# Performance work log

Measured on AMD Instinct MI355X. Metric: run time of the kernel, lower is better.

Reference implementation:

```python
import jax, jax.numpy as jnp
import numpy as np

TAU = 0.2
ALPHA = 0.8
LAM_POS = 1.5  # extrapolation lambda (hard positives)
EPS = 1e-8


def _cosine_sim(e):
    # torch F.cosine_similarity with eps=1e-8 norm clamping
    n = jnp.maximum(jnp.linalg.norm(e, axis=1), EPS)
    return (e @ e.T) / (n[:, None] * n[None, :])


def setup_inputs() -> dict:
    key = jax.random.key(0)
    N, D = 4096, 128
    emb = jax.random.normal(key, (N, D), dtype=jnp.float32)
    k = jnp.arange(N // 2, dtype=jnp.int32)
    i, j = 2 * k, 2 * k + 1
    # disjoint positive pairs, both orientations (matches symmetric set semantics)
    pp = jnp.concatenate([jnp.stack([i, j], 1), jnp.stack([j, i], 1)], 0)
    return {"embeddings": emb, "positive_pairs": pp, "stage_train": 1}


def reference(embeddings, positive_pairs, stage_train):
    N = embeddings.shape[0]
    pi, pj = positive_pairs[:, 0], positive_pairs[:, 1]
    Mp = jnp.zeros((N, N), dtype=bool).at[pi, pj].set(True)  # symmetric (both dirs in pairs)
    eye = jnp.eye(N, dtype=bool)
    Mn = (~eye) & (~Mp)  # negative pair mask

    # hard positive extrapolation: 1.5*e_i - 0.5*e_j (pairs disjoint -> order-free)
    hard_pos = jnp.zeros_like(embeddings).at[pi].set(
        LAM_POS * embeddings[pi] + (1.0 - LAM_POS) * embeddings[pj])

    # hard negative interpolation: loop over negatives in row-major order, last write
    idx = jnp.arange(N, dtype=jnp.int32)
    posmat = idx[:, None] * N + idx[None, :]          # enumeration position of pair (i,j)
    A = jnp.where(Mn, posmat, -1)
    col_max, col_arg = A.max(axis=0), A.argmax(axis=0)  # m as second element of (i,m)
    row_max, row_arg = A.max(axis=1), A.argmax(axis=1)  # m as first element of (m,j)
    partner = jnp.where(col_max > row_max, col_arg, row_arg)
    hard_neg = 0.5 * (embeddings + embeddings[partner])

    sim = _cosine_sim(embeddings)
    sim = jnp.where(Mp, _cosine_sim(hard_pos), jnp.where(Mn, _cosine_sim(hard_neg), sim))

    # contrastive loss with quantile hard mining
    mask = eye | Mp
    exp_sim = jnp.exp(sim / TAU)
    exp_masked = jnp.where(mask, 0.0, exp_sim)
    pos_ij = exp_sim[pi, pj]
    pos_ji = exp_sim[pj, pi]
    ei = exp_masked[pi]  # [2P, N]
    ej = exp_masked[pj]
    if stage_train:
        ti = jnp.quantile(ei, ALPHA, axis=1, keepdims=True)
        tj = jnp.quantile(ej, ALPHA, axis=1, keepdims=True)
        si = jnp.where(ei >= ti, ei, 0.0).sum(axis=1)
        sj = jnp.where(ej >= tj, ej, 0.0).sum(axis=1)
    else:
        si = ei.sum(axis=1)
        sj = ej.sum(axis=1)
    loss_ij = -jnp.log(pos_ij / (pos_ij + si))
    loss_ji = -jnp.log(pos_ji / (pos_ji + sj))
    num_pairs = positive_pairs.shape[0]
    return (loss_ij + loss_ji).sum() / (2 * num_pairs)
```

## Files before the change

### kernel.cpp

```cpp
#include <hip/hip_runtime.h>
#include <hip/hip_bf16.h>
#include <math.h>

#define D 128
#define INV_TAU 5.0f
#define BINS 512
#define BSTRIDE 520
#define CCAP 384

typedef short bf16x8 __attribute__((ext_vector_type(8)));
typedef float f32x4 __attribute__((ext_vector_type(4)));

__global__ void scatter_pos(const int* __restrict__ pp, int* __restrict__ pos,
                            float* __restrict__ out, int K) {
    int k = blockIdx.x * blockDim.x + threadIdx.x;
    if (k == 0) *out = 0.0f;
    if (k < K) pos[pp[2 * k]] = pp[2 * k + 1];
}

__global__ void partner_kernel(const int* __restrict__ pos, int* __restrict__ partner,
                               int N) {
    int r = blockIdx.x * blockDim.x + threadIdx.x;
    if (r >= N) return;
    int posr = pos[r];
    int jmax = -1;
    for (int j = N - 1; j >= 0; --j) {
        if (j != r && j != posr) { jmax = j; break; }
    }
    int imax = -1;
    for (int i = N - 1; i >= 0; --i) {
        if (i != r && pos[i] != r) { imax = i; break; }
    }
    long long rowm = (jmax >= 0) ? (long long)r * N + jmax : -1;
    long long colm = (imax >= 0) ? (long long)imax * N + r : -1;
    partner[r] = (colm > rowm) ? (imax < 0 ? 0 : imax) : (jmax < 0 ? 0 : jmax);
}

__global__ void prep_kernel(const float* __restrict__ emb, const int* __restrict__ partner,
                            const int* __restrict__ pp, __hip_bfloat16* __restrict__ hnn,
                            float* __restrict__ hpn, int N) {
    int b = blockIdx.x, d = threadIdx.x;
    float h;
    int outrow;
    bool isHn = (b < N);
    if (isHn) {
        int p = partner[b];
        h = 0.5f * (emb[b * D + d] + emb[p * D + d]);
        outrow = b;
    } else {
        int k = b - N;
        int a = pp[2 * k], bb = pp[2 * k + 1];
        h = 1.5f * emb[a * D + d] - 0.5f * emb[bb * D + d];
        outrow = a;
    }
    float ss = h * h;
#pragma unroll
    for (int off = 32; off > 0; off >>= 1) ss += __shfl_down(ss, off);
    __shared__ float tmp[2];
    if ((d & 63) == 0) tmp[d >> 6] = ss;
    __syncthreads();
    float inv = 1.0f / fmaxf(sqrtf(tmp[0] + tmp[1]), 1e-8f);
    if (isHn)
        hnn[outrow * D + d] = __float2bfloat16(h * inv);
    else
        hpn[outrow * D + d] = h * inv;
}

__global__ __launch_bounds__(1024, 4) void fused_gram_select(
    const __hip_bfloat16* __restrict__ hnn, const int* __restrict__ pos,
    const int* __restrict__ stage, float* __restrict__ s_out, int N, int q) {
    __shared__ unsigned hist[16 * BSTRIDE];
    __shared__ float rowSum[16];
    __shared__ float tVal_s[16];
    __shared__ int tBin_s[16], tRem_s[16], cCnt[16], pos_s[16];

    int tid = threadIdx.x;
    int wave = tid >> 6, lane = tid & 63;
    int quad = lane >> 4, l15 = lane & 15;
    int rowBase = blockIdx.x * 16;
    int st = stage[0];

    for (int i = tid; i < 16 * BSTRIDE; i += 1024) hist[i] = 0;
    if (tid < 16) {
        rowSum[tid] = 0.0f;
        cCnt[tid] = 0;
        tVal_s[tid] = -1e31f;
        pos_s[tid] = pos[rowBase + tid];
    }
    __syncthreads();

    const short* hs = (const short*)hnn;
    bf16x8 afrag[4];
#pragma unroll
    for (int kk = 0; kk < 4; ++kk)
        afrag[kk] = *(const bf16x8*)&hs[(rowBase + l15) * D + kk * 32 + quad * 8];

    float simv[16][4];
#pragma unroll
    for (int t = 0; t < 16; ++t) {
        int colBase = (wave * 16 + t) * 16;
        bf16x8 bfrag[4];
#pragma unroll
        for (int kk = 0; kk < 4; ++kk)
            bfrag[kk] = *(const bf16x8*)&hs[(colBase + l15) * D + kk * 32 + quad * 8];
        f32x4 acc = {0.f, 0.f, 0.f, 0.f};
#pragma unroll
        for (int kk = 0; kk < 4; ++kk)
            acc = __builtin_amdgcn_mfma_f32_16x16x32_bf16(afrag[kk], bfrag[kk], acc, 0, 0, 0);
        int c = colBase + l15;
#pragma unroll
        for (int rg = 0; rg < 4; ++rg) {
            int rloc = quad * 4 + rg;
            int r = rowBase + rloc;
            float v = acc[rg];
            bool masked = (c == r) || (c == pos_s[rloc]);
            v = masked ? -1e30f : v;
            simv[t][rg] = v;
            if (st) {
                int bin = (int)floorf((v + 1.0f) * (float)(BINS / 2));
                bin = max(0, min(BINS - 1, bin));
                atomicAdd(&hist[rloc * BSTRIDE + bin], 1u);
            }
        }
    }
    __syncthreads();

    if (st) {
        int rloc = wave;
        int base = lane * (BINS / 64);
        unsigned p = 0;
#pragma unroll
        for (int b = 0; b < BINS / 64; ++b) p += hist[rloc * BSTRIDE + base + b];
        unsigned incl = p;
#pragma unroll
        for (int off = 1; off < 64; off <<= 1) {
            unsigned nb = __shfl_up(incl, off);
            if (lane >= off) incl += nb;
        }
        unsigned excl = incl - p;
        unsigned uq = (unsigned)q;
        if (uq >= excl && uq < excl + p) {
            unsigned rem = uq - excl, acc2 = 0;
            int b = 0;
            for (; b < BINS / 64; ++b) {
                unsigned h = hist[rloc * BSTRIDE + base + b];
                if (acc2 + h > rem) break;
                acc2 += h;
            }
            tBin_s[rloc] = base + b;
            tRem_s[rloc] = (int)(rem - acc2);
        }
    } else {
        if (tid < 16) { tBin_s[tid] = -1; tRem_s[tid] = 0; }
    }
    __syncthreads();

    float* cand = (float*)hist;
    float partial[4] = {0.f, 0.f, 0.f, 0.f};
#pragma unroll
    for (int t = 0; t < 16; ++t) {
#pragma unroll
        for (int rg = 0; rg < 4; ++rg) {
            int rloc = quad * 4 + rg;
            float v = simv[t][rg];
            int tb = tBin_s[rloc];
            int bin = 0;
            if (st) {
                bin = (int)floorf((v + 1.0f) * (float)(BINS / 2));
                bin = max(0, min(BINS - 1, bin));
            }
            if (bin > tb) {
                partial[rg] += __expf(v * INV_TAU);
            } else if (bin == tb) {
                int ix = atomicAdd(&cCnt[rloc], 1);
                if (ix < CCAP) cand[rloc * BSTRIDE + ix] = v;
            }
        }
    }
#pragma unroll
    for (int rg = 0; rg < 4; ++rg) {
        float v = partial[rg];
        v += __shfl_xor(v, 1);
        v += __shfl_xor(v, 2);
        v += __shfl_xor(v, 4);
        v += __shfl_xor(v, 8);
        if (l15 == 0) atomicAdd(&rowSum[quad * 4 + rg], v);
    }
    __syncthreads();

    {
        int rloc = wave;
        int m = min(cCnt[rloc], CCAP);
        int rem = tRem_s[rloc];
        for (int i = lane; i < m; i += 64) {
            float v = cand[rloc * BSTRIDE + i];
            int less = 0, eq = 0;
            for (int j = 0; j < m; ++j) {
                float w = cand[rloc * BSTRIDE + j];
                less += (w < v);
                eq += (w == v);
            }
            if (less <= rem && rem < less + eq) tVal_s[rloc] = v;
        }
    }
    __syncthreads();

    {
        int rloc = wave;
        int m = min(cCnt[rloc], CCAP);
        float tv = tVal_s[rloc];
        float csum = 0.0f;
        for (int i = lane; i < m; i += 64) {
            float v = cand[rloc * BSTRIDE + i];
            if (v >= tv) csum += __expf(v * INV_TAU);
        }
#pragma unroll
        for (int off = 1; off < 64; off <<= 1) csum += __shfl_xor(csum, off);
        if (lane == 0) s_out[rowBase + rloc] = rowSum[rloc] + csum;
    }
}

__global__ __launch_bounds__(1024) void loss_kernel(const float* __restrict__ hpn,
                                                    const float* __restrict__ s,
                                                    const int* __restrict__ pp,
                                                    float* __restrict__ out, int K,
                                                    float scale) {
    int wave = threadIdx.x >> 6, lane = threadIdx.x & 63;
    int k = blockIdx.x * 16 + wave;
    float part = 0.0f;
    if (k < K) {
        int a = pp[2 * k], b = pp[2 * k + 1];
        float dsum = hpn[a * D + lane] * hpn[b * D + lane] +
                     hpn[a * D + lane + 64] * hpn[b * D + lane + 64];
#pragma unroll
        for (int off = 32; off > 0; off >>= 1) dsum += __shfl_down(dsum, off);
        if (lane == 0) {
            float p = __expf(dsum * INV_TAU);
            part = log1pf(s[a] / p) + log1pf(s[b] / p);
        }
    }
    __shared__ float red[16];
    if (lane == 0) red[wave] = part;
    __syncthreads();
    if (threadIdx.x == 0) {
        float tot = 0.0f;
#pragma unroll
        for (int w = 0; w < 16; ++w) tot += red[w];
        atomicAdd(out, tot * scale);
    }
}

extern "C" void kernel_launch(void* const* d_in, const int* in_sizes, int n_in,
                              void* d_out, int out_size, void* d_ws, size_t ws_size,
                              hipStream_t stream) {
    const float* emb = (const float*)d_in[0];
    const int* pp = (const int*)d_in[1];
    const int* stage = (const int*)d_in[2];
    int N = in_sizes[0] / D;
    int K = in_sizes[1] / 2;

    char* ws = (char*)d_ws;
    size_t offPos = 0;
    size_t offPartner = offPos + (size_t)N * 4;
    size_t offHnn = offPartner + (size_t)N * 4;
    size_t offHpn = offHnn + (size_t)N * D * 2;
    size_t offS = offHpn + (size_t)N * D * 4;
    int* pos = (int*)(ws + offPos);
    int* partner = (int*)(ws + offPartner);
    __hip_bfloat16* hnn = (__hip_bfloat16*)(ws + offHnn);
    float* hpn = (float*)(ws + offHpn);
    float* s = (float*)(ws + offS);

    scatter_pos<<<(K + 255) / 256, 256, 0, stream>>>(pp, pos, (float*)d_out, K);
    partner_kernel<<<(N + 255) / 256, 256, 0, stream>>>(pos, partner, N);
    prep_kernel<<<N + K, D, 0, stream>>>(emb, partner, pp, hnn, hpn, N);
    int q = (int)(0.8 * (double)(N - 1));
    fused_gram_select<<<N / 16, 1024, 0, stream>>>(hnn, pos, stage, s, N, q);
    loss_kernel<<<(K + 15) / 16, 1024, 0, stream>>>(hpn, s, pp, (float*)d_out, K,
                                                    1.0f / (2.0f * K));
}
```

Baseline: 122.3 us.

## Recompute Gram tiles in two passes instead of caching, fuse partner into prep

The fused Gram/select kernel no longer holds all 64 similarity values per lane in registers. It recomputes the MFMA tiles in a second pass, with software-prefetched B fragments, which lowers register pressure and may raise occupancy. The partner computation moves into prep_kernel, run by one thread per block, which removes a kernel launch and the partner buffer. The cost is doing the MFMA work and hnn loads twice, plus a serial scan on thread 0 of each prep block.

```diff
diff --git a/kernel.cpp b/kernel.cpp
--- a/kernel.cpp
+++ b/kernel.cpp
@@ -11,6 +11,12 @@
 typedef short bf16x8 __attribute__((ext_vector_type(8)));
 typedef float f32x4 __attribute__((ext_vector_type(4)));
 
+__device__ __forceinline__ int bin_of(float v) {
+    float bf = fmaf(v, (float)(BINS / 2), (float)(BINS / 2));
+    bf = fminf(fmaxf(bf, 0.0f), (float)(BINS - 1));
+    return (int)bf;
+}
+
 __global__ void scatter_pos(const int* __restrict__ pp, int* __restrict__ pos,
                             float* __restrict__ out, int K) {
     int k = blockIdx.x * blockDim.x + threadIdx.x;
@@ -18,33 +24,32 @@
     if (k < K) pos[pp[2 * k]] = pp[2 * k + 1];
 }
 
-__global__ void partner_kernel(const int* __restrict__ pos, int* __restrict__ partner,
-                               int N) {
-    int r = blockIdx.x * blockDim.x + threadIdx.x;
-    if (r >= N) return;
-    int posr = pos[r];
-    int jmax = -1;
-    for (int j = N - 1; j >= 0; --j) {
-        if (j != r && j != posr) { jmax = j; break; }
-    }
-    int imax = -1;
-    for (int i = N - 1; i >= 0; --i) {
-        if (i != r && pos[i] != r) { imax = i; break; }
-    }
-    long long rowm = (jmax >= 0) ? (long long)r * N + jmax : -1;
-    long long colm = (imax >= 0) ? (long long)imax * N + r : -1;
-    partner[r] = (colm > rowm) ? (imax < 0 ? 0 : imax) : (jmax < 0 ? 0 : jmax);
-}
-
-__global__ void prep_kernel(const float* __restrict__ emb, const int* __restrict__ partner,
+__global__ void prep_kernel(const float* __restrict__ emb, const int* __restrict__ pos,
                             const int* __restrict__ pp, __hip_bfloat16* __restrict__ hnn,
                             float* __restrict__ hpn, int N) {
     int b = blockIdx.x, d = threadIdx.x;
+    __shared__ int sP;
+    __shared__ float tmp[2];
+    bool isHn = (b < N);
+    if (isHn && d == 0) {
+        int r = b, posr = pos[r];
+        int jmax = -1;
+        for (int j = N - 1; j >= 0; --j) {
+            if (j != r && j != posr) { jmax = j; break; }
+        }
+        int imax = -1;
+        for (int i = N - 1; i >= 0; --i) {
+            if (i != r && pos[i] != r) { imax = i; break; }
+        }
+        long long rowm = (jmax >= 0) ? (long long)r * N + jmax : -1;
+        long long colm = (imax >= 0) ? (long long)imax * N + r : -1;
+        sP = (colm > rowm) ? (imax < 0 ? 0 : imax) : (jmax < 0 ? 0 : jmax);
+    }
+    __syncthreads();
     float h;
     int outrow;
-    bool isHn = (b < N);
     if (isHn) {
-        int p = partner[b];
+        int p = sP;
         h = 0.5f * (emb[b * D + d] + emb[p * D + d]);
         outrow = b;
     } else {
@@ -56,7 +61,6 @@
     float ss = h * h;
 #pragma unroll
     for (int off = 32; off > 0; off >>= 1) ss += __shfl_down(ss, off);
-    __shared__ float tmp[2];
     if ((d & 63) == 0) tmp[d >> 6] = ss;
     __syncthreads();
     float inv = 1.0f / fmaxf(sqrtf(tmp[0] + tmp[1]), 1e-8f);
@@ -80,7 +84,9 @@
     int rowBase = blockIdx.x * 16;
     int st = stage[0];
 
-    for (int i = tid; i < 16 * BSTRIDE; i += 1024) hist[i] = 0;
+    if (st) {
+        for (int i = tid; i < 16 * BSTRIDE; i += 1024) hist[i] = 0;
+    }
     if (tid < 16) {
         rowSum[tid] = 0.0f;
         cCnt[tid] = 0;
@@ -95,60 +101,62 @@
     for (int kk = 0; kk < 4; ++kk)
         afrag[kk] = *(const bf16x8*)&hs[(rowBase + l15) * D + kk * 32 + quad * 8];
 
-    float simv[16][4];
-#pragma unroll
-    for (int t = 0; t < 16; ++t) {
-        int colBase = (wave * 16 + t) * 16;
-        bf16x8 bfrag[4];
-#pragma unroll
-        for (int kk = 0; kk < 4; ++kk)
-            bfrag[kk] = *(const bf16x8*)&hs[(colBase + l15) * D + kk * 32 + quad * 8];
-        f32x4 acc = {0.f, 0.f, 0.f, 0.f};
-#pragma unroll
-        for (int kk = 0; kk < 4; ++kk)
-            acc = __builtin_amdgcn_mfma_f32_16x16x32_bf16(afrag[kk], bfrag[kk], acc, 0, 0, 0);
-        int c = colBase + l15;
-#pragma unroll
-        for (int rg = 0; rg < 4; ++rg) {
-            int rloc = quad * 4 + rg;
-            int r = rowBase + rloc;
-            float v = acc[rg];
-            bool masked = (c == r) || (c == pos_s[rloc]);
-            v = masked ? -1e30f : v;
-            simv[t][rg] = v;
-            if (st) {
-                int bin = (int)floorf((v + 1.0f) * (float)(BINS / 2));
-                bin = max(0, min(BINS - 1, bin));
-                atomicAdd(&hist[rloc * BSTRIDE + bin], 1u);
-            }
-        }
-    }
-    __syncthreads();
+    const short* bp = hs + (size_t)(wave * 256 + l15) * D + quad * 8;
 
     if (st) {
-        int rloc = wave;
-        int base = lane * (BINS / 64);
-        unsigned p = 0;
-#pragma unroll
-        for (int b = 0; b < BINS / 64; ++b) p += hist[rloc * BSTRIDE + base + b];
-        unsigned incl = p;
-#pragma unroll
-        for (int off = 1; off < 64; off <<= 1) {
-            unsigned nb = __shfl_up(incl, off);
-            if (lane >= off) incl += nb;
-        }
-        unsigned excl = incl - p;
-        unsigned uq = (unsigned)q;
-        if (uq >= excl && uq < excl + p) {
-            unsigned rem = uq - excl, acc2 = 0;
-            int b = 0;
-            for (; b < BINS / 64; ++b) {
-                unsigned h = hist[rloc * BSTRIDE + base + b];
-                if (acc2 + h > rem) break;
-                acc2 += h;
-            }
-            tBin_s[rloc] = base + b;
-            tRem_s[rloc] = (int)(rem - acc2);
+        bf16x8 cur[4], nxt[4];
+#pragma unroll
+        for (int kk = 0; kk < 4; ++kk) cur[kk] = *(const bf16x8*)(bp + kk * 32);
+#pragma unroll
+        for (int t = 0; t < 16; ++t) {
+            if (t < 15) {
+                const short* np = bp + (t + 1) * 16 * D;
+#pragma unroll
+                for (int kk = 0; kk < 4; ++kk) nxt[kk] = *(const bf16x8*)(np + kk * 32);
+            }
+            f32x4 acc = {0.f, 0.f, 0.f, 0.f};
+#pragma unroll
+            for (int kk = 0; kk < 4; ++kk)
+                acc = __builtin_amdgcn_mfma_f32_16x16x32_bf16(afrag[kk], cur[kk], acc, 0, 0, 0);
+            int c = wave * 256 + t * 16 + l15;
+#pragma unroll
+            for (int rg = 0; rg < 4; ++rg) {
+                int rloc = quad * 4 + rg;
+                float v = acc[rg];
+                bool masked = (c == rowBase + rloc) || (c == pos_s[rloc]);
+                v = masked ? -1e30f : v;
+                atomicAdd(&hist[rloc * BSTRIDE + bin_of(v)], 1u);
+            }
+#pragma unroll
+            for (int kk = 0; kk < 4; ++kk) cur[kk] = nxt[kk];
+        }
+        __syncthreads();
+
+        {
+            int rloc = wave;
+            int base = lane * (BINS / 64);
+            unsigned p = 0;
+#pragma unroll
+            for (int b = 0; b < BINS / 64; ++b) p += hist[rloc * BSTRIDE + base + b];
+            unsigned incl = p;
+#pragma unroll
+            for (int off = 1; off < 64; off <<= 1) {
+                unsigned nb = __shfl_up(incl, off);
+                if (lane >= off) incl += nb;
+            }
+            unsigned excl = incl - p;
+            unsigned uq = (unsigned)q;
+            if (uq >= excl && uq < excl + p) {
+                unsigned rem = uq - excl, acc2 = 0;
+                int b = 0;
+                for (; b < BINS / 64; ++b) {
+                    unsigned h = hist[rloc * BSTRIDE + base + b];
+                    if (acc2 + h > rem) break;
+                    acc2 += h;
+                }
+                tBin_s[rloc] = base + b;
+                tRem_s[rloc] = (int)(rem - acc2);
+            }
         }
     } else {
         if (tid < 16) { tBin_s[tid] = -1; tRem_s[tid] = 0; }
@@ -156,35 +164,50 @@
     __syncthreads();
 
     float* cand = (float*)hist;
-    float partial[4] = {0.f, 0.f, 0.f, 0.f};
-#pragma unroll
-    for (int t = 0; t < 16; ++t) {
+    {
+        float partial[4] = {0.f, 0.f, 0.f, 0.f};
+        bf16x8 cur[4], nxt[4];
+#pragma unroll
+        for (int kk = 0; kk < 4; ++kk) cur[kk] = *(const bf16x8*)(bp + kk * 32);
+#pragma unroll
+        for (int t = 0; t < 16; ++t) {
+            if (t < 15) {
+                const short* np = bp + (t + 1) * 16 * D;
+#pragma unroll
+                for (int kk = 0; kk < 4; ++kk) nxt[kk] = *(const bf16x8*)(np + kk * 32);
+            }
+            f32x4 acc = {0.f, 0.f, 0.f, 0.f};
+#pragma unroll
+            for (int kk = 0; kk < 4; ++kk)
+                acc = __builtin_amdgcn_mfma_f32_16x16x32_bf16(afrag[kk], cur[kk], acc, 0, 0, 0);
+            int c = wave * 256 + t * 16 + l15;
+#pragma unroll
+            for (int rg = 0; rg < 4; ++rg) {
+                int rloc = quad * 4 + rg;
+                float v = acc[rg];
+                bool masked = (c == rowBase + rloc) || (c == pos_s[rloc]);
+                v = masked ? -1e30f : v;
+                int tb = tBin_s[rloc];
+                int bin = st ? bin_of(v) : 0;
+                if (bin > tb) {
+                    partial[rg] += __expf(v * INV_TAU);
+                } else if (bin == tb) {
+                    int ix = atomicAdd(&cCnt[rloc], 1);
+                    if (ix < CCAP) cand[rloc * BSTRIDE + ix] = v;
+                }
+            }
+#pragma unroll
+            for (int kk = 0; kk < 4; ++kk) cur[kk] = nxt[kk];
+        }
 #pragma unroll
         for (int rg = 0; rg < 4; ++rg) {
-            int rloc = quad * 4 + rg;
-            float v = simv[t][rg];
-            int tb = tBin_s[rloc];
-            int bin = 0;
-            if (st) {
-                bin = (int)floorf((v + 1.0f) * (float)(BINS / 2));
-                bin = max(0, min(BINS - 1, bin));
-            }
-            if (bin > tb) {
-                partial[rg] += __expf(v * INV_TAU);
-            } else if (bin == tb) {
-                int ix = atomicAdd(&cCnt[rloc], 1);
-                if (ix < CCAP) cand[rloc * BSTRIDE + ix] = v;
-            }
-        }
-    }
-#pragma unroll
-    for (int rg = 0; rg < 4; ++rg) {
-        float v = partial[rg];
-        v += __shfl_xor(v, 1);
-        v += __shfl_xor(v, 2);
-        v += __shfl_xor(v, 4);
-        v += __shfl_xor(v, 8);
-        if (l15 == 0) atomicAdd(&rowSum[quad * 4 + rg], v);
+            float v = partial[rg];
+            v += __shfl_xor(v, 1);
+            v += __shfl_xor(v, 2);
+            v += __shfl_xor(v, 4);
+            v += __shfl_xor(v, 8);
+            if (l15 == 0) atomicAdd(&rowSum[quad * 4 + rg], v);
+        }
     }
     __syncthreads();
 
@@ -261,19 +284,16 @@
 
     char* ws = (char*)d_ws;
     size_t offPos = 0;
-    size_t offPartner = offPos + (size_t)N * 4;
-    size_t offHnn = offPartner + (size_t)N * 4;
+    size_t offHnn = offPos + (size_t)N * 4;
     size_t offHpn = offHnn + (size_t)N * D * 2;
     size_t offS = offHpn + (size_t)N * D * 4;
     int* pos = (int*)(ws + offPos);
-    int* partner = (int*)(ws + offPartner);
     __hip_bfloat16* hnn = (__hip_bfloat16*)(ws + offHnn);
     float* hpn = (float*)(ws + offHpn);
     float* s = (float*)(ws + offS);
 
     scatter_pos<<<(K + 255) / 256, 256, 0, stream>>>(pp, pos, (float*)d_out, K);
-    partner_kernel<<<(N + 255) / 256, 256, 0, stream>>>(pos, partner, N);
-    prep_kernel<<<N + K, D, 0, stream>>>(emb, partner, pp, hnn, hpn, N);
+    prep_kernel<<<N + K, D, 0, stream>>>(emb, pos, pp, hnn, hpn, N);
     int q = (int)(0.8 * (double)(N - 1));
     fused_gram_select<<<N / 16, 1024, 0, stream>>>(hnn, pos, stage, s, N, q);
     loss_kernel<<<(K + 15) / 16, 1024, 0, stream>>>(hpn, s, pp, (float*)d_out, K,
```

New measurement: 142.8 us. +16.7%, slower.
